# Kernel tuning notes

Measured on AMD Instinct MI355X. Metric: run time of the kernel, lower is better.

Reference implementation:

```python
import jax, jax.numpy as jnp
import numpy as np
from jax import lax

BEV_SIZE = 250
BEV_RANGE = 50.0
BEV_RES = 0.4
SZ = BEV_SIZE * BEV_SIZE
N_POINTS = 5_000_000
EPS = 1e-5


def setup_inputs() -> dict:
    key = jax.random.key(0)
    ks = jax.random.split(key, 8)
    # points: x,y in [-55,55) (some out of range), z in [-3,5), intensity in [0,1)
    xy = jax.random.uniform(ks[0], (N_POINTS, 2), jnp.float32, -55.0, 55.0)
    z = jax.random.uniform(ks[1], (N_POINTS, 1), jnp.float32, -3.0, 5.0)
    it = jax.random.uniform(ks[2], (N_POINTS, 1), jnp.float32, 0.0, 1.0)
    points = jnp.concatenate([xy, z, it], axis=1)

    def he(k, shape):
        fan_in = shape[1] * shape[2] * shape[3]
        return jax.random.normal(k, shape, jnp.float32) * np.sqrt(2.0 / fan_in)

    return {
        "points": points,
        "w1": he(ks[3], (32, 4, 3, 3)), "b1": jnp.zeros(32), "g1": jnp.ones(32), "beta1": jnp.zeros(32),
        "w2": he(ks[4], (64, 32, 3, 3)), "b2": jnp.zeros(64), "g2": jnp.ones(64), "beta2": jnp.zeros(64),
        "w3": he(ks[5], (64, 64, 3, 3)), "b3": jnp.zeros(64), "g3": jnp.ones(64), "beta3": jnp.zeros(64),
    }


def points_to_bev(points):
    x, y, z, inten = points[:, 0], points[:, 1], points[:, 2], points[:, 3]
    valid = (x >= -BEV_RANGE) & (x < BEV_RANGE) & (y >= -BEV_RANGE) & (y < BEV_RANGE)
    xi = jnp.clip(((x + BEV_RANGE) / BEV_RES).astype(jnp.int32), 0, BEV_SIZE - 1)
    yi = jnp.clip(((y + BEV_RANGE) / BEV_RES).astype(jnp.int32), 0, BEV_SIZE - 1)
    # invalid points routed to an extra dummy bin SZ, sliced off afterwards
    flat = jnp.where(valid, yi * BEV_SIZE + xi, SZ)

    max_z = jnp.full(SZ + 1, -jnp.inf, jnp.float32).at[flat].max(z)[:SZ]
    max_z = jnp.where(jnp.isinf(max_z), 0.0, max_z)
    min_z = jnp.full(SZ + 1, jnp.inf, jnp.float32).at[flat].min(z)[:SZ]
    min_z = jnp.where(jnp.isinf(min_z), 0.0, min_z)
    density = jnp.zeros(SZ + 1, jnp.float32).at[flat].add(1.0)[:SZ]
    isum = jnp.zeros(SZ + 1, jnp.float32).at[flat].add(inten)[:SZ]
    mean_i = jnp.where(density > 0, isum / jnp.maximum(density, 1.0), 0.0)

    bev = jnp.stack([max_z, min_z, jnp.log1p(density), mean_i], axis=0)
    return bev.reshape(4, BEV_SIZE, BEV_SIZE)


def conv_bn_relu(x, w, b, g, beta):
    # x: (1, Cin, H, W), w: (Cout, Cin, 3, 3)
    y = lax.conv_general_dilated(x, w, (1, 1), "SAME",
                                 dimension_numbers=("NCHW", "OIHW", "NCHW"))
    y = y + b[None, :, None, None]
    # BatchNorm2d in training mode: batch stats over (N, H, W)
    mu = jnp.mean(y, axis=(0, 2, 3), keepdims=True)
    var = jnp.mean((y - mu) ** 2, axis=(0, 2, 3), keepdims=True)
    y = (y - mu) * lax.rsqrt(var + EPS)
    y = y * g[None, :, None, None] + beta[None, :, None, None]
    return jax.nn.relu(y)


def reference(points, w1, b1, g1, beta1, w2, b2, g2, beta2, w3, b3, g3, beta3):
    bev = points_to_bev(points)[None]  # (1, 4, 250, 250)
    h = conv_bn_relu(bev, w1, b1, g1, beta1)
    h = conv_bn_relu(h, w2, b2, g2, beta2)
    h = conv_bn_relu(h, w3, b3, g3, beta3)
    return h  # (1, 64, 250, 250)
```

## Files before the change

### kernel.cpp

```cpp
#include <hip/hip_runtime.h>


constexpr int BEVW = 250;
constexpr int SZC  = BEVW * BEVW;
constexpr int NB   = 512;
constexpr int PPT  = 16;
constexpr int CHUNK = 256 * PPT;
constexpr int NBKT = 100;
constexpr int NCELL = 625;
constexpr int CAPB = 43008;
constexpr int NSL  = 8;

__device__ __forceinline__ unsigned f2ord(float f) {
    unsigned u = __float_as_uint(f);
    return (u & 0x80000000u) ? ~u : (u | 0x80000000u);
}
__device__ __forceinline__ float ord2f(unsigned u) {
    unsigned b = (u & 0x80000000u) ? (u & 0x7FFFFFFFu) : ~u;
    return __uint_as_float(b);
}

__global__ void k_initg(unsigned* __restrict__ gcnt) {
    if (threadIdx.x < 128) gcnt[threadIdx.x] = 0u;
}

__launch_bounds__(256)
__global__ void k_bucket(const float4* __restrict__ pts, int n,
                         unsigned long long* __restrict__ recs,
                         unsigned* __restrict__ gcnt) {
    __shared__ unsigned lcnt[NBKT];
    __shared__ unsigned lbase[NBKT];
    const int tid = threadIdx.x;
    if (tid < NBKT) lcnt[tid] = 0u;
    __syncthreads();

    const int ppb = (n + NB - 1) / NB;
    const int start = blockIdx.x * ppb;
    const int end = min(start + ppb, n);

    for (int c0 = start; c0 < end; c0 += CHUNK) {
        unsigned long long rec[PPT];
        int bkt[PPT];
        unsigned slot[PPT];
        unsigned vmask = 0u;
#pragma unroll
        for (int k = 0; k < PPT; ++k) {
            int p = c0 + k * 256 + tid;
            if (p >= end) continue;
            float4 q = pts[p];
            if (!(q.x >= -50.0f && q.x < 50.0f && q.y >= -50.0f && q.y < 50.0f))
                continue;
            int xi = (int)((q.x + 50.0f) / 0.4f);
            int yi = (int)((q.y + 50.0f) / 0.4f);
            xi = min(max(xi, 0), BEVW - 1);
            yi = min(max(yi, 0), BEVW - 1);
            int b  = (yi / 25) * 10 + (xi / 25);
            int cl = (yi % 25) * 25 + (xi % 25);
            unsigned iq = (unsigned)(q.w * 4194304.0f);
            rec[k] = ((unsigned long long)f2ord(q.z) << 32) |
                     ((unsigned long long)(unsigned)cl << 22) | iq;
            bkt[k] = b;
            slot[k] = atomicAdd(&lcnt[b], 1u);
            vmask |= 1u << k;
        }
        __syncthreads();
        if (tid < NBKT) {
            unsigned c = lcnt[tid];
            if (c) lbase[tid] = atomicAdd(&gcnt[tid], c);
            lcnt[tid] = 0u;
        }
        __syncthreads();
#pragma unroll
        for (int k = 0; k < PPT; ++k) {
            if (!((vmask >> k) & 1u)) continue;
            unsigned idx = lbase[bkt[k]] + slot[k];
            if (idx < (unsigned)CAPB)
                recs[(size_t)bkt[k] * CAPB + idx] = rec[k];
        }
    }
}

__launch_bounds__(1024)
__global__ void k_reduce(const unsigned long long* __restrict__ recs,
                         const unsigned* __restrict__ gcnt,
                         float* __restrict__ bev) {
    __shared__ unsigned mxA[NCELL], mnA[NCELL], ctA[NCELL], siA[NCELL];
    const int b = blockIdx.x;
    for (int i = threadIdx.x; i < NCELL; i += 1024) {
        mxA[i] = 0u; mnA[i] = 0xFFFFFFFFu; ctA[i] = 0u; siA[i] = 0u;
    }
    __syncthreads();
    const unsigned nb = min(gcnt[b], (unsigned)CAPB);
    const unsigned long long* rb = recs + (size_t)b * CAPB;
    for (unsigned i = threadIdx.x; i < nb; i += 1024) {
        unsigned long long r = rb[i];
        unsigned zo = (unsigned)(r >> 32);
        unsigned cl = ((unsigned)(r >> 22)) & 0x3FFu;
        unsigned iq = (unsigned)r & 0x3FFFFFu;
        atomicMax(&mxA[cl], zo);
        atomicMin(&mnA[cl], zo);
        atomicAdd(&ctA[cl], 1u);
        atomicAdd(&siA[cl], iq);
    }
    __syncthreads();
    const int tx = b % 10, ty = b / 10;
    for (int i = threadIdx.x; i < NCELL; i += 1024) {
        int cy = ty * 25 + i / 25, cx = tx * 25 + i % 25;
        int cell = cy * BEVW + cx;
        unsigned c = ctA[i];
        bool has = c > 0u;
        float dn = (float)c;
        float isum = (float)siA[i] * (1.0f / 4194304.0f);
        bev[0 * SZC + cell] = has ? ord2f(mxA[i]) : 0.0f;
        bev[1 * SZC + cell] = has ? ord2f(mnA[i]) : 0.0f;
        bev[2 * SZC + cell] = log1pf(dn);
        bev[3 * SZC + cell] = has ? isum / dn : 0.0f;
    }
}

__global__ void k_wt(const float* __restrict__ w, float* __restrict__ wt,
                     int CIN, int COUT) {
    int i = blockIdx.x * blockDim.x + threadIdx.x;
    if (i >= COUT * CIN * 9) return;
    int oc = i / (CIN * 9);
    int r  = i % (CIN * 9);
    int ic = r / 9, k = r % 9;
    wt[(ic * 9 + k) * COUT + oc] = w[i];
}

template <int CIN, int COUT, int ICB, int OCG, bool FUSE>
__launch_bounds__(256)
__global__ void k_conv(const float* __restrict__ in, const float* __restrict__ wt,
                       const float* __restrict__ bias, const float* __restrict__ ab,
                       float* __restrict__ out) {
    __shared__ float s_in[ICB][18 * 18];

    const int tid = threadIdx.x;
    const int u = tid & 15, v = tid >> 4;
    const int tile = blockIdx.x;
    const int tx = (tile & 15) * 16, ty = (tile >> 4) * 16;
    const int oc0 = blockIdx.y * OCG;

    float acc[OCG];
#pragma unroll
    for (int o = 0; o < OCG; ++o) acc[o] = 0.0f;

    for (int ic0 = 0; ic0 < CIN; ic0 += ICB) {
        __syncthreads();
        for (int e = tid; e < ICB * 324; e += 256) {
            int c = e / 324, rem = e % 324;
            int r = rem / 18, q = rem % 18;
            int cg = ic0 + c;
            int gy = ty - 1 + r, gx = tx - 1 + q;
            float x = 0.0f;
            if (gy >= 0 && gy < BEVW && gx >= 0 && gx < BEVW) {
                x = in[(size_t)cg * SZC + gy * BEVW + gx];
                if (FUSE) x = fmaxf(fmaf(x, ab[2 * cg], ab[2 * cg + 1]), 0.0f);
            }
            s_in[c][rem] = x;
        }
        __syncthreads();

#pragma unroll
        for (int icl = 0; icl < ICB; ++icl) {
            const int icg = ic0 + icl;
#pragma unroll
            for (int tap = 0; tap < 9; ++tap) {
                const int ky = tap / 3, kx = tap % 3;
                float x = s_in[icl][(v + ky) * 18 + u + kx];
                const float* wk = wt + ((size_t)(icg * 9 + tap) * COUT + oc0);
#pragma unroll
                for (int o = 0; o < OCG; ++o)
                    acc[o] = fmaf(x, wk[o], acc[o]);
            }
        }
    }

    const int ox = tx + u, oy = ty + v;
    if (ox < BEVW && oy < BEVW) {
#pragma unroll
        for (int o = 0; o < OCG; ++o)
            out[(size_t)(oc0 + o) * SZC + oy * BEVW + ox] = acc[o] + bias[oc0 + o];
    }
}

__global__ void k_bnstats1(const float* __restrict__ y, double* __restrict__ part) {
    const int c = blockIdx.x, s = blockIdx.y;
    const int lo = s * ((SZC + NSL - 1) / NSL);
    const int hi = min(lo + (SZC + NSL - 1) / NSL, SZC);
    const float* p = y + (size_t)c * SZC;
    double sm = 0.0, s2 = 0.0;
    for (int i = lo + threadIdx.x; i < hi; i += 256) {
        float v = p[i];
        sm += (double)v;
        s2 += (double)v * (double)v;
    }
    for (int off = 32; off; off >>= 1) {
        sm += __shfl_down(sm, off);
        s2 += __shfl_down(s2, off);
    }
    __shared__ double sh[8];
    int wid = threadIdx.x >> 6;
    if ((threadIdx.x & 63) == 0) { sh[wid * 2] = sm; sh[wid * 2 + 1] = s2; }
    __syncthreads();
    if (threadIdx.x == 0) {
        double S = 0.0, S2 = 0.0;
        for (int wv = 0; wv < 4; ++wv) { S += sh[wv * 2]; S2 += sh[wv * 2 + 1]; }
        part[(c * NSL + s) * 2]     = S;
        part[(c * NSL + s) * 2 + 1] = S2;
    }
}

__global__ void k_bnstats2(const double* __restrict__ part, const float* __restrict__ g,
                           const float* __restrict__ beta, float* __restrict__ statsAB) {
    int c = threadIdx.x;
    double S = 0.0, S2 = 0.0;
    for (int s = 0; s < NSL; ++s) {
        S  += part[(c * NSL + s) * 2];
        S2 += part[(c * NSL + s) * 2 + 1];
    }
    double mu  = S / (double)SZC;
    double var = S2 / (double)SZC - mu * mu;
    double A = (1.0 / sqrt(var + 1e-5)) * (double)g[c];
    statsAB[2 * c]     = (float)A;
    statsAB[2 * c + 1] = (float)((double)beta[c] - mu * A);
}

__global__ void k_bnreluS(const float* __restrict__ y, const float* __restrict__ ab,
                          float* __restrict__ out) {
    int c = blockIdx.y;
    int i = blockIdx.x * blockDim.x + threadIdx.x;
    if (i >= SZC) return;
    size_t idx = (size_t)c * SZC + i;
    out[idx] = fmaxf(fmaf(y[idx], ab[2 * c], ab[2 * c + 1]), 0.0f);
}

extern "C" void kernel_launch(void* const* d_in, const int* in_sizes, int n_in,
                              void* d_out, int out_size, void* d_ws, size_t ws_size,
                              hipStream_t stream) {
    const float4* pts = (const float4*)d_in[0];
    const float* w1 = (const float*)d_in[1];
    const float* b1 = (const float*)d_in[2];
    const float* g1 = (const float*)d_in[3];
    const float* be1 = (const float*)d_in[4];
    const float* w2 = (const float*)d_in[5];
    const float* b2 = (const float*)d_in[6];
    const float* g2 = (const float*)d_in[7];
    const float* be2 = (const float*)d_in[8];
    const float* w3 = (const float*)d_in[9];
    const float* b3 = (const float*)d_in[10];
    const float* g3 = (const float*)d_in[11];
    const float* be3 = (const float*)d_in[12];

    float* ws = (float*)d_ws;
    const size_t wsf = ws_size / 4;

    constexpr size_t TAILF = 128 + 250000 + 64 + 128 + 128 + 2048 + 1152 + 18432 + 36864;
    float* tail = ws + (wsf - TAILF);
    unsigned* gcnt = (unsigned*)tail;
    float* bev = tail + 128;
    float* st1 = bev + 4 * SZC;
    float* st2 = st1 + 64;
    float* st3 = st2 + 128;
    double* part = (double*)(st3 + 128);
    float* wt1 = st3 + 128 + 2048;
    float* wt2 = wt1 + 1152;
    float* wt3 = wt2 + 18432;

    unsigned long long* recs = (unsigned long long*)ws;
    float* y1 = ws;
    float* y2 = ws + 2000000;
    float* out = (float*)d_out;

    int n = in_sizes[0] / 4;
    const int cellBlocks = (SZC + 255) / 256;

    k_wt<<<(32 * 4 * 9 + 255) / 256, 256, 0, stream>>>(w1, wt1, 4, 32);
    k_wt<<<(64 * 32 * 9 + 255) / 256, 256, 0, stream>>>(w2, wt2, 32, 64);
    k_wt<<<(64 * 64 * 9 + 255) / 256, 256, 0, stream>>>(w3, wt3, 64, 64);

    k_initg<<<1, 128, 0, stream>>>(gcnt);
    k_bucket<<<NB, 256, 0, stream>>>(pts, n, recs, gcnt);
    k_reduce<<<NBKT, 1024, 0, stream>>>(recs, gcnt, bev);

    k_conv<4, 32, 4, 16, false><<<dim3(256, 2), 256, 0, stream>>>(bev, wt1, b1, nullptr, y1);
    k_bnstats1<<<dim3(32, NSL), 256, 0, stream>>>(y1, part);
    k_bnstats2<<<1, 32, 0, stream>>>(part, g1, be1, st1);

    k_conv<32, 64, 8, 16, true><<<dim3(256, 4), 256, 0, stream>>>(y1, wt2, b2, st1, y2);
    k_bnstats1<<<dim3(64, NSL), 256, 0, stream>>>(y2, part);
    k_bnstats2<<<1, 64, 0, stream>>>(part, g2, be2, st2);

    k_conv<64, 64, 8, 16, true><<<dim3(256, 4), 256, 0, stream>>>(y2, wt3, b3, st2, out);
    k_bnstats1<<<dim3(64, NSL), 256, 0, stream>>>(out, part);
    k_bnstats2<<<1, 64, 0, stream>>>(part, g3, be3, st3);

    k_bnreluS<<<dim3(cellBlocks, 64), 256, 0, stream>>>(out, st3, out);
}
```

Measured before the change: 288.5 us.

## Stage bucketed records in shared memory for coalesced bucket-contiguous global writes

The bucketing kernel now prefix-sums the per-block bucket counts and first writes each chunk's records into shared memory, sorted by bucket. Threads then write consecutive positions to global memory, finding each position's bucket by binary search, so stores to each bucket's region are contiguous rather than scattered. Points per thread drop from 16 to 8 to keep the shared staging buffer at 16 KB. The cost is extra barriers, a scan and a binary search per chunk, and half as much work per chunk.

Measured after the change: 301.8 us. 4.6% more time.

```diff
diff --git a/kernel.cpp b/kernel.cpp
--- a/kernel.cpp
+++ b/kernel.cpp
@@ -4,7 +4,7 @@
 constexpr int BEVW = 250;
 constexpr int SZC  = BEVW * BEVW;
 constexpr int NB   = 512;
-constexpr int PPT  = 16;
+constexpr int PPT  = 8;
 constexpr int CHUNK = 256 * PPT;
 constexpr int NBKT = 100;
 constexpr int NCELL = 625;
@@ -28,8 +28,10 @@
 __global__ void k_bucket(const float4* __restrict__ pts, int n,
                          unsigned long long* __restrict__ recs,
                          unsigned* __restrict__ gcnt) {
+    __shared__ unsigned long long recL[CHUNK];
     __shared__ unsigned lcnt[NBKT];
     __shared__ unsigned lbase[NBKT];
+    __shared__ unsigned csum[128];
     const int tid = threadIdx.x;
     if (tid < NBKT) lcnt[tid] = 0u;
     __syncthreads();
@@ -64,19 +66,51 @@
             vmask |= 1u << k;
         }
         __syncthreads();
+
         if (tid < NBKT) {
             unsigned c = lcnt[tid];
-            if (c) lbase[tid] = atomicAdd(&gcnt[tid], c);
-            lcnt[tid] = 0u;
-        }
-        __syncthreads();
+            lbase[tid] = c ? atomicAdd(&gcnt[tid], c) : 0u;
+        }
+        if (tid < 128) csum[tid] = (tid < NBKT) ? lcnt[tid] : 0u;
+        __syncthreads();
+#pragma unroll
+        for (int st = 1; st < 128; st <<= 1) {
+            unsigned add = 0u;
+            if (tid < 128 && tid >= st) add = csum[tid - st];
+            __syncthreads();
+            if (tid < 128) csum[tid] += add;
+            __syncthreads();
+        }
+        const unsigned tot = csum[NBKT - 1];
+
 #pragma unroll
         for (int k = 0; k < PPT; ++k) {
             if (!((vmask >> k) & 1u)) continue;
-            unsigned idx = lbase[bkt[k]] + slot[k];
-            if (idx < (unsigned)CAPB)
-                recs[(size_t)bkt[k] * CAPB + idx] = rec[k];
-        }
+            int b = bkt[k];
+            unsigned pos = csum[b] - lcnt[b] + slot[k];
+            recL[pos] = rec[k];
+        }
+        __syncthreads();
+
+#pragma unroll
+        for (int k = 0; k < PPT; ++k) {
+            unsigned pos = (unsigned)(k * 256 + tid);
+            if (pos < tot) {
+                int lo = 0, hi = NBKT - 1;
+#pragma unroll
+                for (int it = 0; it < 7; ++it) {
+                    int mid = (lo + hi) >> 1;
+                    if (csum[mid] > pos) hi = mid; else lo = mid + 1;
+                }
+                int b = lo;
+                unsigned idx = lbase[b] + pos - (csum[b] - lcnt[b]);
+                if (idx < (unsigned)CAPB)
+                    recs[(size_t)b * CAPB + idx] = recL[pos];
+            }
+        }
+        __syncthreads();
+        if (tid < NBKT) lcnt[tid] = 0u;
+        __syncthreads();
     }
 }
 
```
